# Kernel tuning notes

Hardware: AMD Instinct MI355X
Metric: run time of the kernel (lower is better)

The kernel has to match this reference:

```python
import jax, jax.numpy as jnp
import numpy as np
import math

H = 8                 # num_heads
MAX_REL = 32          # max_relative_distance
VOCAB_REL = 2 * MAX_REL + 1


def setup_inputs() -> dict:
    key = jax.random.key(0)
    ks = jax.random.split(key, 8)
    B, S, D = 4, 2048, 256
    hd = D // H
    sd = 1.0 / math.sqrt(D)
    inp = {
        "query": jax.random.normal(ks[0], (B, S, D), jnp.float32),
        "mask": jnp.ones((B, 1, 1, S), jnp.float32),
        "Wq": jax.random.normal(ks[1], (D, D), jnp.float32) * sd,
        "bq": jnp.zeros((D,), jnp.float32),
        "Wk": jax.random.normal(ks[2], (D, D), jnp.float32) * sd,
        "bk": jnp.zeros((D,), jnp.float32),
        "Wv": jax.random.normal(ks[3], (D, D), jnp.float32) * sd,
        "bv": jnp.zeros((D,), jnp.float32),
        "Wo": jax.random.normal(ks[4], (D, D), jnp.float32) * sd,
        "bo": jnp.zeros((D,), jnp.float32),
        "rel_table": jax.random.normal(ks[5], (VOCAB_REL, hd), jnp.float32) * 0.1,
    }
    return inp


def _split_heads(x, B, S, hd):
    # [B,S,D] -> [B,H,S,hd]
    return x.reshape(B, S, H, hd).transpose(0, 2, 1, 3)


def _relative_row_sums(S, rel_table):
    # Original: emb = table[relpos]  (S,S,hd); scores += einsum('bhid,jkd->bhijk', Q, emb).sum(-1)
    # == einsum('bhid,jd->bhij', Q, R) with R[j,d] = sum_k emb[j,k,d].
    # Compute R without materializing the (S,S,hd) tensor: count how often each
    # relative-position bucket appears in each row, then counts @ table.
    pos = jnp.arange(S)
    relpos = jnp.clip(pos[:, None] - pos[None, :], -MAX_REL, MAX_REL) + MAX_REL  # [S,S] ints
    rows = jnp.broadcast_to(pos[:, None], (S, S))
    counts = jnp.zeros((S, VOCAB_REL), rel_table.dtype).at[
        rows.reshape(-1), relpos.reshape(-1)
    ].add(1.0)
    return counts @ rel_table  # [S, hd]


def reference(query, mask, Wq, bq, Wk, bk, Wv, bv, Wo, bo, rel_table):
    B, S, D = query.shape
    hd = D // H
    scale = 1.0 / math.sqrt(hd)

    Q = _split_heads(query @ Wq + bq, B, S, hd)
    K = _split_heads(query @ Wk + bk, B, S, hd)   # key defaults to query
    V = _split_heads(query @ Wv + bv, B, S, hd)   # value defaults to key

    scores = jnp.einsum("bhid,bhjd->bhij", Q, K) * scale
    R = _relative_row_sums(S, rel_table)          # [S, hd]
    scores = scores + jnp.einsum("bhid,jd->bhij", Q, R)

    scores = scores + (1.0 - mask) * -1e9         # mask broadcast [B,1,1,S]
    attn = jax.nn.softmax(scores, axis=-1)        # dropout is identity (training=False)

    out = jnp.einsum("bhij,bhjd->bhid", attn, V)
    out = out.transpose(0, 2, 1, 3).reshape(B, S, D)
    return out @ Wo + bo
```

## Files before the change

kernel.cpp:

```cpp
#include <hip/hip_runtime.h>
#include <hip/hip_bf16.h>
#include <math.h>

#define NH 8
#define HD 32
#define SEQ 2048
#define DM 256
#define SCALE 0.17677669529663687f
#define INV_SCALE 5.656854249492381f
#define LOG2E 1.4426950408889634f
#define QSC (SCALE * LOG2E)
#define MNEG (-1e9f * LOG2E)

typedef float f32x4 __attribute__((ext_vector_type(4)));
typedef __bf16 bf16x8 __attribute__((ext_vector_type(8)));

#define GLOAD(g, l) __builtin_amdgcn_global_load_lds( \
    (const __attribute__((address_space(1))) void*)(g), \
    (__attribute__((address_space(3))) void*)(l), 16, 0, 0)

__global__ void k_prep(const float* __restrict__ mask,
                       const float* __restrict__ Wq, const float* __restrict__ Wk,
                       const float* __restrict__ Wv, const float* __restrict__ Wo,
                       const float* __restrict__ bq, const float* __restrict__ tbl,
                       __bf16* __restrict__ Wt, __bf16* __restrict__ WoT,
                       float* __restrict__ MT,
                       __bf16* __restrict__ SUFn, __bf16* __restrict__ PREn,
                       float* __restrict__ WV2T, float* __restrict__ cb,
                       int* __restrict__ MFLAG) {
  const int blk = blockIdx.x, tid = threadIdx.x;
  __shared__ float ts[64][65];
  __shared__ int okl;
  if (blk < 64) {
    const int idx = blk;
    const float* W;
    __bf16* dst;
    int tile;
    if (idx < 48) {
      int which = idx >> 4;
      W = which == 0 ? Wq : (which == 1 ? Wk : Wv);
      dst = Wt + which * 65536;
      tile = idx & 15;
    } else {
      W = Wo; dst = WoT; tile = idx - 48;
    }
    const int tr = (tile >> 2) * 64, tc = (tile & 3) * 64;
#pragma unroll
    for (int p = 0; p < 4; ++p) {
      int row = p * 16 + (tid >> 4);
      int col = (tid & 15) * 4;
      float4 v = *(const float4*)(W + (size_t)(tr + row) * 256 + tc + col);
      ts[row][col] = v.x; ts[row][col + 1] = v.y;
      ts[row][col + 2] = v.z; ts[row][col + 3] = v.w;
    }
    __syncthreads();
#pragma unroll
    for (int p = 0; p < 2; ++p) {
      int n = p * 32 + (tid >> 3);
      int kb = (tid & 7) * 8;
      union { __bf16 h[8]; bf16x8 v; } o;
#pragma unroll
      for (int e = 0; e < 8; ++e) o.h[e] = (__bf16)ts[kb + e][n];
      *(bf16x8*)(dst + (size_t)(tc + n) * 256 + tr + kb) = o.v;
    }
  } else if (blk == 64) {
    if (tid == 0) okl = 1;
    __syncthreads();
    bool ok = true;
    for (int i = tid; i < 4 * SEQ; i += 256) {
      float mv = mask[i];
      MT[i] = (1.0f - mv) * MNEG;
      ok &= (mv == 1.0f);
    }
    if (!ok) atomicAnd(&okl, 0);
    __syncthreads();
    if (tid == 0) MFLAG[0] = okl;
  } else if (blk == 65) {
    for (int idx = tid; idx < 1024; idx += 256) {
      int j = idx >> 5, d = idx & 31;
      float s = 0.f;
      for (int u = j + 33; u <= 63; ++u) s += tbl[u * 32 + d];
      SUFn[idx] = (__bf16)(-s * INV_SCALE);
    }
    for (int idx = tid; idx < 1024; idx += 256) {
      int jj = idx >> 5, d = idx & 31;
      float s = 0.f;
      for (int u = 1; u <= jj; ++u) s += tbl[u * 32 + d];
      PREn[idx] = (__bf16)(-s * INV_SCALE);
    }
  } else if (blk < 82) {
    int tg = (blk - 66) * 256 + tid;
    int hv = tg >> 8, k = tg & 255;
    const float* T = tbl + ((hv & 1) ? 0 : 64 * 32);
    const float* w = Wq + (size_t)k * 256 + (hv >> 1) * 32;
    float acc = 0.f;
#pragma unroll
    for (int d = 0; d < 32; ++d) acc = fmaf(w[d], T[d], acc);
    WV2T[hv * 256 + k] = acc * LOG2E;
  } else {
    if (tid < 16) {
      const float* T = tbl + ((tid & 1) ? 0 : 64 * 32);
      float a = 0.f;
#pragma unroll
      for (int d = 0; d < 32; ++d) a = fmaf(bq[(tid >> 1) * 32 + d], T[d], a);
      cb[tid] = a * LOG2E;
    }
  }
}

__launch_bounds__(256)
__global__ void k_rel(const float* __restrict__ X, const float* __restrict__ WV2T,
                      const float* __restrict__ cb, float* __restrict__ REL,
                      __bf16* __restrict__ Xb) {
  __shared__ float Xs[32][260];
  __shared__ float Ws[16][260];
  const int tid = threadIdx.x;
  const size_t base = (size_t)blockIdx.x * 32 * 256;
#pragma unroll
  for (int p = 0; p < 8; ++p) {
    int idx = p * 1024 + tid * 4;
    float4 v = *(const float4*)(X + base + idx);
    *(float4*)&Xs[idx >> 8][idx & 255] = v;
  }
#pragma unroll
  for (int p = 0; p < 4; ++p) {
    int idx = p * 1024 + tid * 4;
    float4 v = *(const float4*)(WV2T + idx);
    *(float4*)&Ws[idx >> 8][idx & 255] = v;
  }
  __syncthreads();
#pragma unroll
  for (int p = 0; p < 4; ++p) {
    int idx = p * 2048 + tid * 8;
    int row = idx >> 8, col = idx & 255;
    float4 a = *(const float4*)&Xs[row][col];
    float4 b4 = *(const float4*)&Xs[row][col + 4];
    union { __bf16 h[8]; bf16x8 v; } o;
    o.h[0] = (__bf16)a.x;  o.h[1] = (__bf16)a.y;
    o.h[2] = (__bf16)a.z;  o.h[3] = (__bf16)a.w;
    o.h[4] = (__bf16)b4.x; o.h[5] = (__bf16)b4.y;
    o.h[6] = (__bf16)b4.z; o.h[7] = (__bf16)b4.w;
    *(bf16x8*)(Xb + base + idx) = o.v;
  }
  const int hv = tid & 15, rl = tid >> 4;
  float a0 = cb[hv], a1 = a0;
  const float* xs0 = &Xs[rl][0];
  const float* xs1 = &Xs[rl + 16][0];
  const float* wsp = &Ws[hv][0];
#pragma unroll 8
  for (int k = 0; k < 256; ++k) {
    float w = wsp[k];
    a0 = fmaf(xs0[k], w, a0);
    a1 = fmaf(xs1[k], w, a1);
  }
  const int row0 = blockIdx.x * 32 + rl;
  const int h = hv >> 1, v = hv & 1;
  const int b0i = row0 >> 11, s0 = row0 & 2047;
  REL[((size_t)(b0i * NH + h) * SEQ + s0) * 2 + v] = a0;
  const int r1 = row0 + 16;
  const int b1i = r1 >> 11, s1 = r1 & 2047;
  REL[((size_t)(b1i * NH + h) * SEQ + s1) * 2 + v] = a1;
}

template <int MODE>
__launch_bounds__(256)
__global__ void k_gemm(const __bf16* __restrict__ A, const __bf16* __restrict__ Bt,
                       const float* __restrict__ b0, const float* __restrict__ b1,
                       const float* __restrict__ b2,
                       __bf16* __restrict__ Qb, __bf16* __restrict__ Kb,
                       __bf16* __restrict__ VTout, float* __restrict__ Y) {
  constexpr int BM = (MODE == 0) ? 128 : 64;
  constexpr int FI = BM / 32;
  __shared__ __align__(16) __bf16 As[BM * 64];
  __shared__ __align__(16) __bf16 Bs[64 * 64];
  const int tid = threadIdx.x, lane = tid & 63, wid = tid >> 6;
  const int l16 = lane & 15, lhi = lane >> 4;
  const int wr = wid >> 1, wc = wid & 1;
  const int m0 = blockIdx.x * BM, n0 = blockIdx.y * 64;

  f32x4 acc[FI][2];
#pragma unroll
  for (int i = 0; i < FI; ++i)
#pragma unroll
    for (int j = 0; j < 2; ++j) acc[i][j] = (f32x4){0.f, 0.f, 0.f, 0.f};

  for (int k0 = 0; k0 < 256; k0 += 64) {
    __syncthreads();
#pragma unroll
    for (int cc = 0; cc < BM / 32; ++cc) {
      int cl = tid + cc * 256;
      int row = cl >> 3, kc = cl & 7;
      int k = k0 + ((kc ^ (row & 7)) * 8);
      const __bf16* src;
      if constexpr (MODE == 0) {
        src = A + (size_t)(m0 + row) * 256 + k;
      } else {
        int r = m0 + row, bb = r >> 11, s = r & 2047, h = k >> 5, dh = k & 31;
        src = A + ((size_t)(bb * NH + h) * SEQ + s) * HD + dh;
      }
      GLOAD(src, (__bf16*)As + (size_t)cl * 8);
    }
#pragma unroll
    for (int cc = 0; cc < 2; ++cc) {
      int cl = tid + cc * 256;
      int row = cl >> 3, kc = cl & 7;
      int k = k0 + ((kc ^ (row & 7)) * 8);
      GLOAD(Bt + (size_t)(n0 + row) * 256 + k, (__bf16*)Bs + (size_t)cl * 8);
    }
    __syncthreads();
#pragma unroll
    for (int kk = 0; kk < 64; kk += 32) {
      bf16x8 af[FI], bfr[2];
#pragma unroll
      for (int fi = 0; fi < FI; ++fi) {
        int row = wr * (BM / 2) + fi * 16 + l16;
        af[fi] = *(const bf16x8*)(As + row * 64 + ((((kk >> 3) + lhi) ^ (row & 7)) * 8));
      }
#pragma unroll
      for (int fj = 0; fj < 2; ++fj) {
        int row = wc * 32 + fj * 16 + l16;
        bfr[fj] = *(const bf16x8*)(Bs + row * 64 + ((((kk >> 3) + lhi) ^ (row & 7)) * 8));
      }
#pragma unroll
      for (int fi = 0; fi < FI; ++fi)
#pragma unroll
        for (int fj = 0; fj < 2; ++fj)
          acc[fi][fj] = __builtin_amdgcn_mfma_f32_16x16x32_bf16(af[fi], bfr[fj], acc[fi][fj], 0, 0, 0);
    }
  }
#pragma unroll
  for (int fi = 0; fi < FI; ++fi) {
#pragma unroll
    for (int fj = 0; fj < 2; ++fj) {
      int mrow = m0 + wr * (BM / 2) + fi * 16 + lhi * 4;
      int ncol = n0 + wc * 32 + fj * 16 + l16;
      if constexpr (MODE == 0) {
        int which = ncol >> 8, nw = ncol & 255, h = nw >> 5, dh = nw & 31;
        int bb = mrow >> 11, s0 = mrow & 2047;
        if (which == 2) {
          union { __bf16 h4[4]; uint2 u; } o;
#pragma unroll
          for (int r = 0; r < 4; ++r) o.h4[r] = (__bf16)(acc[fi][fj][r] + b2[nw]);
          *(uint2*)(VTout + ((size_t)(bb * NH + h) * HD + dh) * SEQ + s0) = o.u;
        } else {
          const float* bias = which == 0 ? b0 : b1;
#pragma unroll
          for (int r = 0; r < 4; ++r) {
            float v = acc[fi][fj][r] + bias[nw];
            size_t oi = ((size_t)(bb * NH + h) * SEQ + (s0 + r)) * HD + dh;
            if (which == 0) Qb[oi] = (__bf16)(v * QSC);
            else Kb[oi] = (__bf16)v;
          }
        }
      } else {
#pragma unroll
        for (int r = 0; r < 4; ++r)
          Y[(size_t)(mrow + r) * 256 + ncol] = acc[fi][fj][r] + b0[ncol];
      }
    }
  }
}

__launch_bounds__(512, 4)
__global__ void k_flash(const __bf16* __restrict__ Qb, const __bf16* __restrict__ Kb,
                        const __bf16* __restrict__ VT, const float* __restrict__ REL,
                        const __bf16* __restrict__ SUFn, const __bf16* __restrict__ PREn,
                        const float* __restrict__ MT, const int* __restrict__ MFLAG,
                        __bf16* __restrict__ Ob) {
  const int bid = blockIdx.x;
  const int bh = (bid & 7) * 4 + ((bid >> 3) & 3);
  const int qt = bid >> 5;
  const int b = bh >> 3;
  const int tid = threadIdx.x, wid = tid >> 6, lane = tid & 63;
  const int l16 = lane & 15, lhi = lane >> 4;

  __shared__ __align__(16) __bf16 kbuf[2][128 * 32];
  __shared__ __align__(16) __bf16 vbuf[2][32 * 128];
  __shared__ __align__(16) __bf16 plds[8][16 * 64];

  const int qrow = qt * 128 + wid * 16 + l16;
  const size_t rg = (size_t)bh * SEQ + qrow;
  const bf16x8 qfrag = *(const bf16x8*)(Qb + rg * HD + lhi * 8);
  const float2 uw = *(const float2*)(REL + rg * 2);
  const float uu = uw.x, ww = uw.y, duw = uu - ww;
  const float duw128 = 128.f * duw;
  const int flag = MFLAG[0];

  f32x4 c0[8];
  {
    const f32x4 cr = {(float)(lhi * 4) * duw, (float)(lhi * 4 + 1) * duw,
                      (float)(lhi * 4 + 2) * duw, (float)(lhi * 4 + 3) * duw};
#pragma unroll
    for (int jt = 0; jt < 8; ++jt)
      c0[jt] = cr + (float)(jt * 16) * duw;
  }

  const int kj = tid >> 2, kc = tid & 3;
  const __bf16* ksrc = Kb + ((size_t)bh * SEQ + kj) * HD + ((kc ^ ((kj >> 1) & 3)) * 8);
  const int vd = tid >> 4, vc = tid & 15;
  const __bf16* vsrc = VT + ((size_t)bh * HD + vd) * SEQ + ((vc ^ (vd & 7)) * 8);

  f32x4 of0 = {0.f, 0.f, 0.f, 0.f}, of1 = {0.f, 0.f, 0.f, 0.f}, of2 = {0.f, 0.f, 0.f, 0.f};
  bf16x8 ones;
#pragma unroll
  for (int e = 0; e < 8; ++e) ones[e] = (__bf16)1.0f;
  float m = -3.0e38f;
  __bf16* pl = &plds[wid][0];
  const float* mtp = MT + b * SEQ + lhi * 4;

  GLOAD(ksrc, &kbuf[0][(size_t)tid * 8]);
  GLOAD(vsrc, &vbuf[0][(size_t)tid * 8]);
  __syncthreads();

  for (int t = 0, cur = 0; t < 16; ++t, cur ^= 1) {
    const int jb = t * 128;
    if (t < 15) {
      GLOAD(ksrc + (size_t)(jb + 128) * HD, &kbuf[cur ^ 1][(size_t)tid * 8]);
      GLOAD(vsrc + (jb + 128), &vbuf[cur ^ 1][(size_t)tid * 8]);
    }
    const __bf16* kb = kbuf[cur];
    const __bf16* vb = vbuf[cur];

    f32x4 sf[8];
    __builtin_amdgcn_s_setprio(1);
#pragma unroll
    for (int jt = 0; jt < 8; ++jt) {
      const int row = jt * 16 + l16;
      bf16x8 kf = *(const bf16x8*)(kb + row * 32 + ((lhi ^ ((row >> 1) & 3)) * 8));
      sf[jt] = __builtin_amdgcn_mfma_f32_16x16x32_bf16(kf, qfrag, c0[jt], 0, 0, 0);
    }
    __builtin_amdgcn_s_setprio(0);

    if (t == 0) {
      const bf16x8 s0 = *(const bf16x8*)(SUFn + l16 * HD + lhi * 8);
      const bf16x8 s1 = *(const bf16x8*)(SUFn + (16 + l16) * HD + lhi * 8);
      sf[0] = __builtin_amdgcn_mfma_f32_16x16x32_bf16(s0, qfrag, sf[0], 0, 0, 0);
      sf[1] = __builtin_amdgcn_mfma_f32_16x16x32_bf16(s1, qfrag, sf[1], 0, 0, 0);
#pragma unroll
      for (int jt = 0; jt < 2; ++jt)
#pragma unroll
        for (int r = 0; r < 4; ++r)
          sf[jt][r] += fmaxf(31.f - (float)(jt * 16 + lhi * 4 + r), 0.f) * uu;
    }
    if (t == 15) {
      const bf16x8 p0 = *(const bf16x8*)(PREn + l16 * HD + lhi * 8);
      const bf16x8 p1 = *(const bf16x8*)(PREn + (16 + l16) * HD + lhi * 8);
      sf[6] = __builtin_amdgcn_mfma_f32_16x16x32_bf16(p0, qfrag, sf[6], 0, 0, 0);
      sf[7] = __builtin_amdgcn_mfma_f32_16x16x32_bf16(p1, qfrag, sf[7], 0, 0, 0);
#pragma unroll
      for (int jt = 6; jt < 8; ++jt)
#pragma unroll
        for (int r = 0; r < 4; ++r)
          sf[jt][r] += fmaxf((float)(jb + jt * 16 + lhi * 4 + r) - 2016.f, 0.f) * ww;
    }
    if (!flag) {
#pragma unroll
      for (int jt = 0; jt < 8; ++jt)
        sf[jt] += *(const f32x4*)(mtp + jb + jt * 16);
    }

    const float tsp = (float)jb * duw; (void)duw128;
    float tmax = -3.0e38f;
#pragma unroll
    for (int jt = 0; jt < 8; ++jt)
      tmax = fmaxf(fmaxf(fmaxf(fmaxf(tmax, sf[jt].x), sf[jt].y), sf[jt].z), sf[jt].w);
    tmax = fmaxf(tmax, __shfl_xor(tmax, 16));
    tmax = fmaxf(tmax, __shfl_xor(tmax, 32));
    const float mn = fmaxf(m, tmax + tsp);
    const float c = __builtin_amdgcn_exp2f(m - mn);
    m = mn;
    const float m2 = mn - tsp;
    of0 *= c; of1 *= c; of2 *= c;

#pragma unroll
    for (int ph = 0; ph < 2; ++ph) {
#pragma unroll
      for (int jt = ph * 4; jt < ph * 4 + 4; ++jt) {
        union { __bf16 h4[4]; uint2 u; } pk;
#pragma unroll
        for (int r = 0; r < 4; ++r)
          pk.h4[r] = (__bf16)__builtin_amdgcn_exp2f(sf[jt][r] - m2);
        const int blk16 = (((jt & 3) * 2 + (lhi >> 1)) ^ (l16 & 7));
        *(uint2*)(pl + l16 * 64 + blk16 * 8 + (lhi & 1) * 4) = pk.u;
      }
      __builtin_amdgcn_s_setprio(1);
#pragma unroll
      for (int kt = ph * 2; kt < ph * 2 + 2; ++kt) {
        const int pblk = (((kt & 1) * 4 + lhi) ^ (l16 & 7));
        bf16x8 pf = *(const bf16x8*)(pl + l16 * 64 + pblk * 8);
        bf16x8 v0 = *(const bf16x8*)(vb + l16 * 128 + (((kt * 4 + lhi) ^ (l16 & 7)) * 8));
        bf16x8 v1 = *(const bf16x8*)(vb + (16 + l16) * 128 + (((kt * 4 + lhi) ^ (l16 & 7)) * 8));
        of0 = __builtin_amdgcn_mfma_f32_16x16x32_bf16(v0, pf, of0, 0, 0, 0);
        of1 = __builtin_amdgcn_mfma_f32_16x16x32_bf16(v1, pf, of1, 0, 0, 0);
        of2 = __builtin_amdgcn_mfma_f32_16x16x32_bf16(ones, pf, of2, 0, 0, 0);
      }
      __builtin_amdgcn_s_setprio(0);
    }
    __syncthreads();
  }

  const float inv = 1.0f / of2[0];
  union { __bf16 h4[4]; uint2 u; } o0, o1;
#pragma unroll
  for (int r = 0; r < 4; ++r) {
    o0.h4[r] = (__bf16)(of0[r] * inv);
    o1.h4[r] = (__bf16)(of1[r] * inv);
  }
  *(uint2*)(Ob + rg * HD + lhi * 4) = o0.u;
  *(uint2*)(Ob + rg * HD + 16 + lhi * 4) = o1.u;
}

extern "C" void kernel_launch(void* const* d_in, const int* in_sizes, int n_in,
                              void* d_out, int out_size, void* d_ws, size_t ws_size,
                              hipStream_t stream) {
  (void)in_sizes; (void)n_in; (void)out_size; (void)ws_size;
  const float* query = (const float*)d_in[0];
  const float* mask  = (const float*)d_in[1];
  const float* Wq = (const float*)d_in[2];
  const float* bq = (const float*)d_in[3];
  const float* Wk = (const float*)d_in[4];
  const float* bk = (const float*)d_in[5];
  const float* Wv = (const float*)d_in[6];
  const float* bv = (const float*)d_in[7];
  const float* Wo = (const float*)d_in[8];
  const float* bo = (const float*)d_in[9];
  const float* tbl = (const float*)d_in[10];
  float* out = (float*)d_out;
  char* ws = (char*)d_ws;

  const size_t MB = 1024ull * 1024;
  __bf16* Xb    = (__bf16*)(ws);
  __bf16* Wt    = (__bf16*)(ws + 4 * MB);
  __bf16* WoT   = (__bf16*)(ws + 4 * MB + 393216);
  __bf16* SUFn  = (__bf16*)(ws + 4 * MB + 524288);
  __bf16* PREn  = (__bf16*)(ws + 4 * MB + 526336);
  float*  WV2T  = (float*) (ws + 4 * MB + 528384);
  float*  cbv   = (float*) (ws + 4 * MB + 544768);
  float*  MT    = (float*) (ws + 4 * MB + 544832);
  int*    MFLAG = (int*)   (ws + 4 * MB + 577600);
  float*  REL   = (float*) (ws + 5 * MB);
  __bf16* Qb    = (__bf16*)(ws + 6 * MB);
  __bf16* Kb    = (__bf16*)(ws + 10 * MB);
  __bf16* VT    = (__bf16*)(ws + 14 * MB);
  __bf16* Ob    = (__bf16*)(ws + 18 * MB);

  k_prep<<<83, 256, 0, stream>>>(mask, Wq, Wk, Wv, Wo, bq, tbl,
                                 Wt, WoT, MT, SUFn, PREn, WV2T, cbv, MFLAG);
  k_rel<<<256, 256, 0, stream>>>(query, WV2T, cbv, REL, Xb);
  k_gemm<0><<<dim3(64, 12), 256, 0, stream>>>(Xb, Wt, bq, bk, bv, Qb, Kb, VT, nullptr);
  k_flash<<<512, 512, 0, stream>>>(Qb, Kb, VT, REL, SUFn, PREn, MT, MFLAG, Ob);
  k_gemm<1><<<dim3(128, 4), 256, 0, stream>>>(Ob, WoT, bo, nullptr, nullptr,
                                              nullptr, nullptr, nullptr, out);
}
```

Measured before the change: 91.64 us.

## Split flash attention over key halves and merge partials in a combine kernel

The attention kernel now splits the key sequence into two halves, launching twice as many blocks. Each block writes unnormalized fp32 partial outputs plus its running max and sum, and a new combine kernel rescales and merges the two halves into the bf16 output. The P tile in LDS shrinks and the PV loop is restructured into four phases, with the linear relative-position term computed incrementally per tile instead of precomputed. This is meant to raise occupancy and parallelism, at the cost of an extra kernel launch and roughly 16MB of fp32 partial traffic.

Result: slower. 103.9 us (+13.4%).

```diff
diff --git a/kernel.cpp b/kernel.cpp
--- a/kernel.cpp
+++ b/kernel.cpp
@@ -11,6 +11,7 @@
 #define LOG2E 1.4426950408889634f
 #define QSC (SCALE * LOG2E)
 #define MNEG (-1e9f * LOG2E)
+#define NROWS (32 * SEQ)
 
 typedef float f32x4 __attribute__((ext_vector_type(4)));
 typedef __bf16 bf16x8 __attribute__((ext_vector_type(8)));
@@ -266,34 +267,28 @@
                         const __bf16* __restrict__ VT, const float* __restrict__ REL,
                         const __bf16* __restrict__ SUFn, const __bf16* __restrict__ PREn,
                         const float* __restrict__ MT, const int* __restrict__ MFLAG,
-                        __bf16* __restrict__ Ob) {
+                        float* __restrict__ OFP, float2* __restrict__ ML) {
   const int bid = blockIdx.x;
-  const int bh = (bid & 7) * 4 + ((bid >> 3) & 3);
-  const int qt = bid >> 5;
+  const int xcd = bid & 7, idx = bid >> 3;
+  const int bh = xcd * 4 + (idx & 3);
+  const int qs = idx >> 2;
+  const int qt = qs & 15, sp = qs >> 4;
   const int b = bh >> 3;
   const int tid = threadIdx.x, wid = tid >> 6, lane = tid & 63;
   const int l16 = lane & 15, lhi = lane >> 4;
 
   __shared__ __align__(16) __bf16 kbuf[2][128 * 32];
   __shared__ __align__(16) __bf16 vbuf[2][32 * 128];
-  __shared__ __align__(16) __bf16 plds[8][16 * 64];
+  __shared__ __align__(16) __bf16 plds[8][16 * 32];
 
   const int qrow = qt * 128 + wid * 16 + l16;
   const size_t rg = (size_t)bh * SEQ + qrow;
   const bf16x8 qfrag = *(const bf16x8*)(Qb + rg * HD + lhi * 8);
   const float2 uw = *(const float2*)(REL + rg * 2);
   const float uu = uw.x, ww = uw.y, duw = uu - ww;
-  const float duw128 = 128.f * duw;
+  const float duw16 = 16.f * duw;
+  const f32x4 duwr = {0.f, duw, 2.f * duw, 3.f * duw};
   const int flag = MFLAG[0];
-
-  f32x4 c0[8];
-  {
-    const f32x4 cr = {(float)(lhi * 4) * duw, (float)(lhi * 4 + 1) * duw,
-                      (float)(lhi * 4 + 2) * duw, (float)(lhi * 4 + 3) * duw};
-#pragma unroll
-    for (int jt = 0; jt < 8; ++jt)
-      c0[jt] = cr + (float)(jt * 16) * duw;
-  }
 
   const int kj = tid >> 2, kc = tid & 3;
   const __bf16* ksrc = Kb + ((size_t)bh * SEQ + kj) * HD + ((kc ^ ((kj >> 1) & 3)) * 8);
@@ -308,26 +303,30 @@
   __bf16* pl = &plds[wid][0];
   const float* mtp = MT + b * SEQ + lhi * 4;
 
-  GLOAD(ksrc, &kbuf[0][(size_t)tid * 8]);
-  GLOAD(vsrc, &vbuf[0][(size_t)tid * 8]);
+  const int t0 = sp * 8;
+  GLOAD(ksrc + (size_t)t0 * 4096, &kbuf[0][(size_t)tid * 8]);
+  GLOAD(vsrc + t0 * 128, &vbuf[0][(size_t)tid * 8]);
   __syncthreads();
 
-  for (int t = 0, cur = 0; t < 16; ++t, cur ^= 1) {
+  for (int tt = 0, cur = 0; tt < 8; ++tt, cur ^= 1) {
+    const int t = t0 + tt;
     const int jb = t * 128;
-    if (t < 15) {
-      GLOAD(ksrc + (size_t)(jb + 128) * HD, &kbuf[cur ^ 1][(size_t)tid * 8]);
-      GLOAD(vsrc + (jb + 128), &vbuf[cur ^ 1][(size_t)tid * 8]);
+    if (tt < 7) {
+      GLOAD(ksrc + (size_t)(t + 1) * 4096, &kbuf[cur ^ 1][(size_t)tid * 8]);
+      GLOAD(vsrc + (t + 1) * 128, &vbuf[cur ^ 1][(size_t)tid * 8]);
     }
     const __bf16* kb = kbuf[cur];
     const __bf16* vb = vbuf[cur];
 
+    f32x4 lin = duwr + (float)(jb + lhi * 4) * duw;
     f32x4 sf[8];
     __builtin_amdgcn_s_setprio(1);
 #pragma unroll
     for (int jt = 0; jt < 8; ++jt) {
       const int row = jt * 16 + l16;
       bf16x8 kf = *(const bf16x8*)(kb + row * 32 + ((lhi ^ ((row >> 1) & 3)) * 8));
-      sf[jt] = __builtin_amdgcn_mfma_f32_16x16x32_bf16(kf, qfrag, c0[jt], 0, 0, 0);
+      sf[jt] = __builtin_amdgcn_mfma_f32_16x16x32_bf16(kf, qfrag, lin, 0, 0, 0);
+      lin += duw16;
     }
     __builtin_amdgcn_s_setprio(0);
 
@@ -359,35 +358,34 @@
         sf[jt] += *(const f32x4*)(mtp + jb + jt * 16);
     }
 
-    const float tsp = (float)jb * duw; (void)duw128;
     float tmax = -3.0e38f;
 #pragma unroll
     for (int jt = 0; jt < 8; ++jt)
       tmax = fmaxf(fmaxf(fmaxf(fmaxf(tmax, sf[jt].x), sf[jt].y), sf[jt].z), sf[jt].w);
     tmax = fmaxf(tmax, __shfl_xor(tmax, 16));
     tmax = fmaxf(tmax, __shfl_xor(tmax, 32));
-    const float mn = fmaxf(m, tmax + tsp);
+    const float mn = fmaxf(m, tmax);
     const float c = __builtin_amdgcn_exp2f(m - mn);
     m = mn;
-    const float m2 = mn - tsp;
     of0 *= c; of1 *= c; of2 *= c;
 
 #pragma unroll
-    for (int ph = 0; ph < 2; ++ph) {
-#pragma unroll
-      for (int jt = ph * 4; jt < ph * 4 + 4; ++jt) {
+    for (int ph = 0; ph < 4; ++ph) {
+#pragma unroll
+      for (int jl = 0; jl < 2; ++jl) {
+        const int jt = ph * 2 + jl;
         union { __bf16 h4[4]; uint2 u; } pk;
 #pragma unroll
         for (int r = 0; r < 4; ++r)
-          pk.h4[r] = (__bf16)__builtin_amdgcn_exp2f(sf[jt][r] - m2);
-        const int blk16 = (((jt & 3) * 2 + (lhi >> 1)) ^ (l16 & 7));
-        *(uint2*)(pl + l16 * 64 + blk16 * 8 + (lhi & 1) * 4) = pk.u;
+          pk.h4[r] = (__bf16)__builtin_amdgcn_exp2f(sf[jt][r] - m);
+        const int blk4 = (jl * 2 + (lhi >> 1)) ^ (l16 & 3);
+        *(uint2*)(pl + l16 * 32 + blk4 * 8 + (lhi & 1) * 4) = pk.u;
       }
       __builtin_amdgcn_s_setprio(1);
-#pragma unroll
-      for (int kt = ph * 2; kt < ph * 2 + 2; ++kt) {
-        const int pblk = (((kt & 1) * 4 + lhi) ^ (l16 & 7));
-        bf16x8 pf = *(const bf16x8*)(pl + l16 * 64 + pblk * 8);
+      {
+        const int kt = ph;
+        const int pblk = lhi ^ (l16 & 3);
+        bf16x8 pf = *(const bf16x8*)(pl + l16 * 32 + pblk * 8);
         bf16x8 v0 = *(const bf16x8*)(vb + l16 * 128 + (((kt * 4 + lhi) ^ (l16 & 7)) * 8));
         bf16x8 v1 = *(const bf16x8*)(vb + (16 + l16) * 128 + (((kt * 4 + lhi) ^ (l16 & 7)) * 8));
         of0 = __builtin_amdgcn_mfma_f32_16x16x32_bf16(v0, pf, of0, 0, 0, 0);
@@ -399,15 +397,30 @@
     __syncthreads();
   }
 
-  const float inv = 1.0f / of2[0];
-  union { __bf16 h4[4]; uint2 u; } o0, o1;
-#pragma unroll
-  for (int r = 0; r < 4; ++r) {
-    o0.h4[r] = (__bf16)(of0[r] * inv);
-    o1.h4[r] = (__bf16)(of1[r] * inv);
-  }
-  *(uint2*)(Ob + rg * HD + lhi * 4) = o0.u;
-  *(uint2*)(Ob + rg * HD + 16 + lhi * 4) = o1.u;
+  float* op = OFP + ((size_t)sp * NROWS + rg) * HD;
+  *(f32x4*)(op + lhi * 4) = of0;
+  *(f32x4*)(op + 16 + lhi * 4) = of1;
+  if (lhi == 0) ML[(size_t)sp * NROWS + rg] = (float2){m, of2[0]};
+}
+
+__launch_bounds__(256)
+__global__ void k_comb(const float* __restrict__ OFP, const float2* __restrict__ ML,
+                       __bf16* __restrict__ Ob) {
+  const int tid = threadIdx.x;
+  const int row = blockIdx.x * 32 + (tid >> 3);
+  const int d = (tid & 7) * 4;
+  const float2 ml0 = ML[row], ml1 = ML[NROWS + row];
+  const float m = fmaxf(ml0.x, ml1.x);
+  const float w0 = __builtin_amdgcn_exp2f(ml0.x - m);
+  const float w1 = __builtin_amdgcn_exp2f(ml1.x - m);
+  const float inv = 1.0f / (ml0.y * w0 + ml1.y * w1);
+  const f32x4 a = *(const f32x4*)(OFP + (size_t)row * HD + d);
+  const f32x4 b4 = *(const f32x4*)(OFP + ((size_t)NROWS + row) * HD + d);
+  union { __bf16 h4[4]; uint2 u; } o;
+#pragma unroll
+  for (int r = 0; r < 4; ++r)
+    o.h4[r] = (__bf16)((a[r] * w0 + b4[r] * w1) * inv);
+  *(uint2*)(Ob + (size_t)row * HD + d) = o.u;
 }
 
 extern "C" void kernel_launch(void* const* d_in, const int* in_sizes, int n_in,
@@ -443,12 +456,15 @@
   __bf16* Kb    = (__bf16*)(ws + 10 * MB);
   __bf16* VT    = (__bf16*)(ws + 14 * MB);
   __bf16* Ob    = (__bf16*)(ws + 18 * MB);
+  float*  OFP   = (float*) (ws + 22 * MB);
+  float2* ML    = (float2*)(ws + 38 * MB);
 
   k_prep<<<83, 256, 0, stream>>>(mask, Wq, Wk, Wv, Wo, bq, tbl,
                                  Wt, WoT, MT, SUFn, PREn, WV2T, cbv, MFLAG);
   k_rel<<<256, 256, 0, stream>>>(query, WV2T, cbv, REL, Xb);
   k_gemm<0><<<dim3(64, 12), 256, 0, stream>>>(Xb, Wt, bq, bk, bv, Qb, Kb, VT, nullptr);
-  k_flash<<<512, 512, 0, stream>>>(Qb, Kb, VT, REL, SUFn, PREn, MT, MFLAG, Ob);
+  k_flash<<<1024, 512, 0, stream>>>(Qb, Kb, VT, REL, SUFn, PREn, MT, MFLAG, OFP, ML);
+  k_comb<<<2048, 256, 0, stream>>>(OFP, ML, Ob);
   k_gemm<1><<<dim3(128, 4), 256, 0, stream>>>(Ob, WoT, bo, nullptr, nullptr,
                                               nullptr, nullptr, nullptr, out);
 }
```

## Process two query row tiles per wave in flash kernel with 256-thread blocks

Applied to the files above, without the earlier changes.

Each wave now handles 32 query rows (two 16-row MFMA tiles) instead of 16, so K and V fragments read from LDS feed two MFMAs each, and the block shrinks to 4 waves with each thread issuing two async loads per tile. The linear relative bias is folded in as an incrementing accumulator initialiser, so the max no longer needs a per-tile offset. This roughly doubles accumulator and score registers per thread and lowers resident waves per CU, trading latency hiding for more instruction-level parallelism and fewer LDS reads.

Result: slower. 110.7 us (+20.8%).

```diff
diff --git a/kernel.cpp b/kernel.cpp
--- a/kernel.cpp
+++ b/kernel.cpp
@@ -261,7 +261,7 @@
   }
 }
 
-__launch_bounds__(512, 4)
+__launch_bounds__(256, 3)
 __global__ void k_flash(const __bf16* __restrict__ Qb, const __bf16* __restrict__ Kb,
                         const __bf16* __restrict__ VT, const float* __restrict__ REL,
                         const __bf16* __restrict__ SUFn, const __bf16* __restrict__ PREn,
@@ -276,138 +276,178 @@
 
   __shared__ __align__(16) __bf16 kbuf[2][128 * 32];
   __shared__ __align__(16) __bf16 vbuf[2][32 * 128];
-  __shared__ __align__(16) __bf16 plds[8][16 * 64];
-
-  const int qrow = qt * 128 + wid * 16 + l16;
-  const size_t rg = (size_t)bh * SEQ + qrow;
-  const bf16x8 qfrag = *(const bf16x8*)(Qb + rg * HD + lhi * 8);
-  const float2 uw = *(const float2*)(REL + rg * 2);
-  const float uu = uw.x, ww = uw.y, duw = uu - ww;
-  const float duw128 = 128.f * duw;
+  __shared__ __align__(16) __bf16 plds[4][2][16 * 64];
+
+  const int qrow0 = qt * 128 + wid * 32 + l16;
+  const size_t rg0 = (size_t)bh * SEQ + qrow0;
+  const size_t rg1 = rg0 + 16;
+  const bf16x8 qfrag0 = *(const bf16x8*)(Qb + rg0 * HD + lhi * 8);
+  const bf16x8 qfrag1 = *(const bf16x8*)(Qb + rg1 * HD + lhi * 8);
+  const float2 uw0 = *(const float2*)(REL + rg0 * 2);
+  const float2 uw1 = *(const float2*)(REL + rg1 * 2);
+  const float duw0 = uw0.x - uw0.y, duw1 = uw1.x - uw1.y;
+  const float d16_0 = 16.f * duw0, d16_1 = 16.f * duw1;
+  const f32x4 dr0 = {0.f, duw0, 2.f * duw0, 3.f * duw0};
+  const f32x4 dr1 = {0.f, duw1, 2.f * duw1, 3.f * duw1};
   const int flag = MFLAG[0];
 
-  f32x4 c0[8];
-  {
-    const f32x4 cr = {(float)(lhi * 4) * duw, (float)(lhi * 4 + 1) * duw,
-                      (float)(lhi * 4 + 2) * duw, (float)(lhi * 4 + 3) * duw};
-#pragma unroll
-    for (int jt = 0; jt < 8; ++jt)
-      c0[jt] = cr + (float)(jt * 16) * duw;
-  }
-
-  const int kj = tid >> 2, kc = tid & 3;
-  const __bf16* ksrc = Kb + ((size_t)bh * SEQ + kj) * HD + ((kc ^ ((kj >> 1) & 3)) * 8);
-  const int vd = tid >> 4, vc = tid & 15;
-  const __bf16* vsrc = VT + ((size_t)bh * HD + vd) * SEQ + ((vc ^ (vd & 7)) * 8);
-
-  f32x4 of0 = {0.f, 0.f, 0.f, 0.f}, of1 = {0.f, 0.f, 0.f, 0.f}, of2 = {0.f, 0.f, 0.f, 0.f};
+  const int u1 = tid + 256;
+  const int kj0 = tid >> 2, kc0 = tid & 3, kj1 = u1 >> 2, kc1 = u1 & 3;
+  const __bf16* ksrc0 = Kb + ((size_t)bh * SEQ + kj0) * HD + ((kc0 ^ ((kj0 >> 1) & 3)) * 8);
+  const __bf16* ksrc1 = Kb + ((size_t)bh * SEQ + kj1) * HD + ((kc1 ^ ((kj1 >> 1) & 3)) * 8);
+  const int vd0 = tid >> 4, vc0 = tid & 15, vd1 = u1 >> 4, vc1 = u1 & 15;
+  const __bf16* vsrc0 = VT + ((size_t)bh * HD + vd0) * SEQ + ((vc0 ^ (vd0 & 7)) * 8);
+  const __bf16* vsrc1 = VT + ((size_t)bh * HD + vd1) * SEQ + ((vc1 ^ (vd1 & 7)) * 8);
+
+  f32x4 oA0 = {0.f, 0.f, 0.f, 0.f}, oA1 = {0.f, 0.f, 0.f, 0.f}, oA2 = {0.f, 0.f, 0.f, 0.f};
+  f32x4 oB0 = {0.f, 0.f, 0.f, 0.f}, oB1 = {0.f, 0.f, 0.f, 0.f}, oB2 = {0.f, 0.f, 0.f, 0.f};
   bf16x8 ones;
 #pragma unroll
   for (int e = 0; e < 8; ++e) ones[e] = (__bf16)1.0f;
-  float m = -3.0e38f;
-  __bf16* pl = &plds[wid][0];
+  float m0 = -3.0e38f, m1 = -3.0e38f;
+  __bf16* pl0 = &plds[wid][0][0];
+  __bf16* pl1 = &plds[wid][1][0];
   const float* mtp = MT + b * SEQ + lhi * 4;
 
-  GLOAD(ksrc, &kbuf[0][(size_t)tid * 8]);
-  GLOAD(vsrc, &vbuf[0][(size_t)tid * 8]);
+  GLOAD(ksrc0, &kbuf[0][(size_t)tid * 8]);
+  GLOAD(ksrc1, &kbuf[0][(size_t)u1 * 8]);
+  GLOAD(vsrc0, &vbuf[0][(size_t)tid * 8]);
+  GLOAD(vsrc1, &vbuf[0][(size_t)u1 * 8]);
   __syncthreads();
 
   for (int t = 0, cur = 0; t < 16; ++t, cur ^= 1) {
     const int jb = t * 128;
     if (t < 15) {
-      GLOAD(ksrc + (size_t)(jb + 128) * HD, &kbuf[cur ^ 1][(size_t)tid * 8]);
-      GLOAD(vsrc + (jb + 128), &vbuf[cur ^ 1][(size_t)tid * 8]);
+      const int nb = cur ^ 1;
+      GLOAD(ksrc0 + (size_t)(jb + 128) * HD, &kbuf[nb][(size_t)tid * 8]);
+      GLOAD(ksrc1 + (size_t)(jb + 128) * HD, &kbuf[nb][(size_t)u1 * 8]);
+      GLOAD(vsrc0 + (jb + 128), &vbuf[nb][(size_t)tid * 8]);
+      GLOAD(vsrc1 + (jb + 128), &vbuf[nb][(size_t)u1 * 8]);
     }
     const __bf16* kb = kbuf[cur];
     const __bf16* vb = vbuf[cur];
 
-    f32x4 sf[8];
+    f32x4 lin0 = dr0 + (float)(jb + lhi * 4) * duw0;
+    f32x4 lin1 = dr1 + (float)(jb + lhi * 4) * duw1;
+    f32x4 sf0[8], sf1[8];
     __builtin_amdgcn_s_setprio(1);
 #pragma unroll
     for (int jt = 0; jt < 8; ++jt) {
       const int row = jt * 16 + l16;
       bf16x8 kf = *(const bf16x8*)(kb + row * 32 + ((lhi ^ ((row >> 1) & 3)) * 8));
-      sf[jt] = __builtin_amdgcn_mfma_f32_16x16x32_bf16(kf, qfrag, c0[jt], 0, 0, 0);
+      sf0[jt] = __builtin_amdgcn_mfma_f32_16x16x32_bf16(kf, qfrag0, lin0, 0, 0, 0);
+      sf1[jt] = __builtin_amdgcn_mfma_f32_16x16x32_bf16(kf, qfrag1, lin1, 0, 0, 0);
+      lin0 += d16_0;
+      lin1 += d16_1;
     }
     __builtin_amdgcn_s_setprio(0);
 
     if (t == 0) {
       const bf16x8 s0 = *(const bf16x8*)(SUFn + l16 * HD + lhi * 8);
       const bf16x8 s1 = *(const bf16x8*)(SUFn + (16 + l16) * HD + lhi * 8);
-      sf[0] = __builtin_amdgcn_mfma_f32_16x16x32_bf16(s0, qfrag, sf[0], 0, 0, 0);
-      sf[1] = __builtin_amdgcn_mfma_f32_16x16x32_bf16(s1, qfrag, sf[1], 0, 0, 0);
+      sf0[0] = __builtin_amdgcn_mfma_f32_16x16x32_bf16(s0, qfrag0, sf0[0], 0, 0, 0);
+      sf0[1] = __builtin_amdgcn_mfma_f32_16x16x32_bf16(s1, qfrag0, sf0[1], 0, 0, 0);
+      sf1[0] = __builtin_amdgcn_mfma_f32_16x16x32_bf16(s0, qfrag1, sf1[0], 0, 0, 0);
+      sf1[1] = __builtin_amdgcn_mfma_f32_16x16x32_bf16(s1, qfrag1, sf1[1], 0, 0, 0);
 #pragma unroll
       for (int jt = 0; jt < 2; ++jt)
 #pragma unroll
-        for (int r = 0; r < 4; ++r)
-          sf[jt][r] += fmaxf(31.f - (float)(jt * 16 + lhi * 4 + r), 0.f) * uu;
+        for (int r = 0; r < 4; ++r) {
+          const float cf = fmaxf(31.f - (float)(jt * 16 + lhi * 4 + r), 0.f);
+          sf0[jt][r] += cf * uw0.x;
+          sf1[jt][r] += cf * uw1.x;
+        }
     }
     if (t == 15) {
       const bf16x8 p0 = *(const bf16x8*)(PREn + l16 * HD + lhi * 8);
       const bf16x8 p1 = *(const bf16x8*)(PREn + (16 + l16) * HD + lhi * 8);
-      sf[6] = __builtin_amdgcn_mfma_f32_16x16x32_bf16(p0, qfrag, sf[6], 0, 0, 0);
-      sf[7] = __builtin_amdgcn_mfma_f32_16x16x32_bf16(p1, qfrag, sf[7], 0, 0, 0);
+      sf0[6] = __builtin_amdgcn_mfma_f32_16x16x32_bf16(p0, qfrag0, sf0[6], 0, 0, 0);
+      sf0[7] = __builtin_amdgcn_mfma_f32_16x16x32_bf16(p1, qfrag0, sf0[7], 0, 0, 0);
+      sf1[6] = __builtin_amdgcn_mfma_f32_16x16x32_bf16(p0, qfrag1, sf1[6], 0, 0, 0);
+      sf1[7] = __builtin_amdgcn_mfma_f32_16x16x32_bf16(p1, qfrag1, sf1[7], 0, 0, 0);
 #pragma unroll
       for (int jt = 6; jt < 8; ++jt)
 #pragma unroll
-        for (int r = 0; r < 4; ++r)
-          sf[jt][r] += fmaxf((float)(jb + jt * 16 + lhi * 4 + r) - 2016.f, 0.f) * ww;
+        for (int r = 0; r < 4; ++r) {
+          const float cf = fmaxf((float)(jb + jt * 16 + lhi * 4 + r) - 2016.f, 0.f);
+          sf0[jt][r] += cf * uw0.y;
+          sf1[jt][r] += cf * uw1.y;
+        }
     }
     if (!flag) {
 #pragma unroll
-      for (int jt = 0; jt < 8; ++jt)
-        sf[jt] += *(const f32x4*)(mtp + jb + jt * 16);
-    }
-
-    const float tsp = (float)jb * duw; (void)duw128;
-    float tmax = -3.0e38f;
-#pragma unroll
-    for (int jt = 0; jt < 8; ++jt)
-      tmax = fmaxf(fmaxf(fmaxf(fmaxf(tmax, sf[jt].x), sf[jt].y), sf[jt].z), sf[jt].w);
-    tmax = fmaxf(tmax, __shfl_xor(tmax, 16));
-    tmax = fmaxf(tmax, __shfl_xor(tmax, 32));
-    const float mn = fmaxf(m, tmax + tsp);
-    const float c = __builtin_amdgcn_exp2f(m - mn);
-    m = mn;
-    const float m2 = mn - tsp;
-    of0 *= c; of1 *= c; of2 *= c;
+      for (int jt = 0; jt < 8; ++jt) {
+        const f32x4 mt4 = *(const f32x4*)(mtp + jb + jt * 16);
+        sf0[jt] += mt4;
+        sf1[jt] += mt4;
+      }
+    }
+
+    float t0x = -3.0e38f, t1x = -3.0e38f;
+#pragma unroll
+    for (int jt = 0; jt < 8; ++jt) {
+      t0x = fmaxf(fmaxf(fmaxf(fmaxf(t0x, sf0[jt].x), sf0[jt].y), sf0[jt].z), sf0[jt].w);
+      t1x = fmaxf(fmaxf(fmaxf(fmaxf(t1x, sf1[jt].x), sf1[jt].y), sf1[jt].z), sf1[jt].w);
+    }
+    t0x = fmaxf(t0x, __shfl_xor(t0x, 16));
+    t0x = fmaxf(t0x, __shfl_xor(t0x, 32));
+    t1x = fmaxf(t1x, __shfl_xor(t1x, 16));
+    t1x = fmaxf(t1x, __shfl_xor(t1x, 32));
+    const float mn0 = fmaxf(m0, t0x), mn1 = fmaxf(m1, t1x);
+    const float c0 = __builtin_amdgcn_exp2f(m0 - mn0);
+    const float c1 = __builtin_amdgcn_exp2f(m1 - mn1);
+    m0 = mn0; m1 = mn1;
+    oA0 *= c0; oA1 *= c0; oA2 *= c0;
+    oB0 *= c1; oB1 *= c1; oB2 *= c1;
 
 #pragma unroll
     for (int ph = 0; ph < 2; ++ph) {
 #pragma unroll
       for (int jt = ph * 4; jt < ph * 4 + 4; ++jt) {
-        union { __bf16 h4[4]; uint2 u; } pk;
-#pragma unroll
-        for (int r = 0; r < 4; ++r)
-          pk.h4[r] = (__bf16)__builtin_amdgcn_exp2f(sf[jt][r] - m2);
+        union { __bf16 h4[4]; uint2 u; } pk0, pk1;
+#pragma unroll
+        for (int r = 0; r < 4; ++r) {
+          pk0.h4[r] = (__bf16)__builtin_amdgcn_exp2f(sf0[jt][r] - m0);
+          pk1.h4[r] = (__bf16)__builtin_amdgcn_exp2f(sf1[jt][r] - m1);
+        }
         const int blk16 = (((jt & 3) * 2 + (lhi >> 1)) ^ (l16 & 7));
-        *(uint2*)(pl + l16 * 64 + blk16 * 8 + (lhi & 1) * 4) = pk.u;
+        *(uint2*)(pl0 + l16 * 64 + blk16 * 8 + (lhi & 1) * 4) = pk0.u;
+        *(uint2*)(pl1 + l16 * 64 + blk16 * 8 + (lhi & 1) * 4) = pk1.u;
       }
       __builtin_amdgcn_s_setprio(1);
 #pragma unroll
       for (int kt = ph * 2; kt < ph * 2 + 2; ++kt) {
         const int pblk = (((kt & 1) * 4 + lhi) ^ (l16 & 7));
-        bf16x8 pf = *(const bf16x8*)(pl + l16 * 64 + pblk * 8);
+        bf16x8 pf0 = *(const bf16x8*)(pl0 + l16 * 64 + pblk * 8);
+        bf16x8 pf1 = *(const bf16x8*)(pl1 + l16 * 64 + pblk * 8);
         bf16x8 v0 = *(const bf16x8*)(vb + l16 * 128 + (((kt * 4 + lhi) ^ (l16 & 7)) * 8));
         bf16x8 v1 = *(const bf16x8*)(vb + (16 + l16) * 128 + (((kt * 4 + lhi) ^ (l16 & 7)) * 8));
-        of0 = __builtin_amdgcn_mfma_f32_16x16x32_bf16(v0, pf, of0, 0, 0, 0);
-        of1 = __builtin_amdgcn_mfma_f32_16x16x32_bf16(v1, pf, of1, 0, 0, 0);
-        of2 = __builtin_amdgcn_mfma_f32_16x16x32_bf16(ones, pf, of2, 0, 0, 0);
+        oA0 = __builtin_amdgcn_mfma_f32_16x16x32_bf16(v0, pf0, oA0, 0, 0, 0);
+        oA1 = __builtin_amdgcn_mfma_f32_16x16x32_bf16(v1, pf0, oA1, 0, 0, 0);
+        oA2 = __builtin_amdgcn_mfma_f32_16x16x32_bf16(ones, pf0, oA2, 0, 0, 0);
+        oB0 = __builtin_amdgcn_mfma_f32_16x16x32_bf16(v0, pf1, oB0, 0, 0, 0);
+        oB1 = __builtin_amdgcn_mfma_f32_16x16x32_bf16(v1, pf1, oB1, 0, 0, 0);
+        oB2 = __builtin_amdgcn_mfma_f32_16x16x32_bf16(ones, pf1, oB2, 0, 0, 0);
       }
       __builtin_amdgcn_s_setprio(0);
     }
     __syncthreads();
   }
 
-  const float inv = 1.0f / of2[0];
-  union { __bf16 h4[4]; uint2 u; } o0, o1;
+  const float inv0 = 1.0f / oA2[0];
+  const float inv1 = 1.0f / oB2[0];
+  union { __bf16 h4[4]; uint2 u; } w0, w1, w2, w3;
 #pragma unroll
   for (int r = 0; r < 4; ++r) {
-    o0.h4[r] = (__bf16)(of0[r] * inv);
-    o1.h4[r] = (__bf16)(of1[r] * inv);
-  }
-  *(uint2*)(Ob + rg * HD + lhi * 4) = o0.u;
-  *(uint2*)(Ob + rg * HD + 16 + lhi * 4) = o1.u;
+    w0.h4[r] = (__bf16)(oA0[r] * inv0);
+    w1.h4[r] = (__bf16)(oA1[r] * inv0);
+    w2.h4[r] = (__bf16)(oB0[r] * inv1);
+    w3.h4[r] = (__bf16)(oB1[r] * inv1);
+  }
+  *(uint2*)(Ob + rg0 * HD + lhi * 4) = w0.u;
+  *(uint2*)(Ob + rg0 * HD + 16 + lhi * 4) = w1.u;
+  *(uint2*)(Ob + rg1 * HD + lhi * 4) = w2.u;
+  *(uint2*)(Ob + rg1 * HD + 16 + lhi * 4) = w3.u;
 }
 
 extern "C" void kernel_launch(void* const* d_in, const int* in_sizes, int n_in,
@@ -448,7 +488,7 @@
                                  Wt, WoT, MT, SUFn, PREn, WV2T, cbv, MFLAG);
   k_rel<<<256, 256, 0, stream>>>(query, WV2T, cbv, REL, Xb);
   k_gemm<0><<<dim3(64, 12), 256, 0, stream>>>(Xb, Wt, bq, bk, bv, Qb, Kb, VT, nullptr);
-  k_flash<<<512, 512, 0, stream>>>(Qb, Kb, VT, REL, SUFn, PREn, MT, MFLAG, Ob);
+  k_flash<<<512, 256, 0, stream>>>(Qb, Kb, VT, REL, SUFn, PREn, MT, MFLAG, Ob);
   k_gemm<1><<<dim3(128, 4), 256, 0, stream>>>(Ob, WoT, bo, nullptr, nullptr,
                                               nullptr, nullptr, nullptr, out);
 }
```
